# Kernel optimization log

Measured on AMD Instinct MI355X. Metric: run time of the kernel, lower is better.

The kernel has to match this reference:

```python
import jax, jax.numpy as jnp
import numpy as np

B, M, E, H, A = 32, 512, 256, 8, 64


def setup_inputs() -> dict:
    key = jax.random.key(0)
    k0, k1, k2, k3, k4 = jax.random.split(key, 5)
    s = 1.0 / np.sqrt(E)
    x = jax.random.normal(k0, (B, M, E), dtype=jnp.float32)
    Wq = jax.random.normal(k1, (E, H * A), dtype=jnp.float32) * s
    Wk = jax.random.normal(k2, (E, H * A), dtype=jnp.float32) * s
    Wv = jax.random.normal(k3, (E, H * A), dtype=jnp.float32) * s
    Wr = jax.random.normal(k4, (E, A), dtype=jnp.float32) * s
    return {"x": x, "Wq": Wq, "Wk": Wk, "Wv": Wv, "Wr": Wr}


def reference(x, Wq, Wk, Wv, Wr):
    # Faithful to the original: (B, M, H*A) tensors are view()'d directly to
    # (H, B, M, A) / (H, B, A, M) without any transpose — this mixes batch
    # into the head axis exactly as the torch code does.
    q = (x @ Wq).reshape(H, B, M, A)   # query view
    k = (x @ Wk).reshape(H, B, A, M)   # keys viewed pre-transposed
    v = (x @ Wv).reshape(H, B, M, A)
    scores = jnp.einsum('hbma,hban->hbmn', q, k)      # (H, B, M, M)
    att = jax.nn.softmax(scores, axis=-1)
    out = jnp.einsum('hbmn,hbna->hbma', att, v)       # (H, B, M, A)
    out = out.mean(axis=0)                            # head-mean -> (B, M, A)
    return jax.nn.relu(out + x @ Wr)
```

## Files before the change

### kernel.cpp

```cpp
#include <hip/hip_runtime.h>
#include <math.h>


typedef _Float16 f16;
typedef _Float16 f16x2 __attribute__((ext_vector_type(2)));
typedef _Float16 f16x4 __attribute__((ext_vector_type(4)));
typedef _Float16 f16x8 __attribute__((ext_vector_type(8)));
typedef float    f32x4 __attribute__((ext_vector_type(4)));

typedef __attribute__((address_space(1))) const void* gas_t;
typedef __attribute__((address_space(3))) void* las_t;

__device__ __forceinline__ void gload16(const void* g, void* l) {
  __builtin_amdgcn_global_load_lds((gas_t)g, (las_t)l, 16, 0, 0);
}

__global__ __launch_bounds__(256) void k_cast(const float* __restrict__ in,
                                              f16* __restrict__ out, int n4) {
  int i = blockIdx.x * 256 + threadIdx.x;
  if (i < n4) {
    f32x4 v = reinterpret_cast<const f32x4*>(in)[i];
    f16x4 h;
    h[0] = (f16)v[0]; h[1] = (f16)v[1]; h[2] = (f16)v[2]; h[3] = (f16)v[3];
    reinterpret_cast<f16x4*>(out)[i] = h;
  }
}

__global__ __launch_bounds__(256) void k_transpose_w(const float* __restrict__ Wq,
                                                     const float* __restrict__ Wk,
                                                     const float* __restrict__ Wv,
                                                     const float* __restrict__ Wr,
                                                     f16* __restrict__ Wt,
                                                     f16* __restrict__ Wrt) {
  __shared__ f16 tile[64][68];
  int b = blockIdx.x;
  const float* src; f16* dst; int r0, c0, Cin;
  if (b < 96) {
    int ws = b >> 5, rem = b & 31;
    src = (ws == 0) ? Wq : (ws == 1) ? Wk : Wv;
    dst = Wt + ws * 512 * 256;
    Cin = 512; r0 = (rem >> 3) * 64; c0 = (rem & 7) * 64;
  } else {
    src = Wr; dst = Wrt; Cin = 64; r0 = (b - 96) * 64; c0 = 0;
  }
  int t = threadIdx.x;
#pragma unroll
  for (int u = 0; u < 8; ++u) {
    int e = u * 256 + t;
    int r = e >> 5, c = (e & 31) << 1;
    const float* p = src + (long)(r0 + r) * Cin + (c0 + c);
    f16x2 v; v[0] = (f16)p[0]; v[1] = (f16)p[1];
    *reinterpret_cast<f16x2*>(&tile[r][c]) = v;
  }
  __syncthreads();
#pragma unroll
  for (int u = 0; u < 16; ++u) {
    int f = u * 256 + t;
    int cc = f >> 6, rr = f & 63;
    dst[(long)(c0 + cc) * 256 + (r0 + rr)] = tile[rr][cc];
  }
}

__global__ __launch_bounds__(256) void k_transpose(const f16* __restrict__ in,
                                                   f16* __restrict__ out,
                                                   int R_, int C_) {
  __shared__ f16 tile[64][68];
  int g = blockIdx.x;
  long gb = (long)g * R_ * C_;
  int r0 = blockIdx.y * 64, c0 = blockIdx.z * 64;
  int t = threadIdx.x;
#pragma unroll
  for (int u = 0; u < 8; ++u) {
    int e = u * 256 + t;
    int r = e >> 5, c = (e & 31) << 1;
    const f16* p = in + gb + (long)(r0 + r) * C_ + (c0 + c);
    f16x2 v; v[0] = p[0]; v[1] = p[1];
    *reinterpret_cast<f16x2*>(&tile[r][c]) = v;
  }
  __syncthreads();
#pragma unroll
  for (int u = 0; u < 16; ++u) {
    int f = u * 256 + t;
    int cc = f >> 6, rr = f & 63;
    out[gb + (long)(c0 + cc) * R_ + (r0 + rr)] = tile[rr][cc];
  }
}

template <int BN, bool F32OUT>
__global__ __launch_bounds__(256, 3) void k_gemm(const f16* __restrict__ Xh,
                                                 const f16* __restrict__ Wt,
                                                 f16* __restrict__ outH,
                                                 float* __restrict__ outF, int N) {
  __shared__ f16 Ash[128 * 64];
  __shared__ f16 Bsh[BN * 64];
  constexpr int NT = BN / 32;
  int t = threadIdx.x;
  int w = t >> 6, l = t & 63;
  int lrow = l & 15, lg = l >> 4;
  int wm = w >> 1, wn = w & 1;
  int rb = blockIdx.x * 128, cb = blockIdx.y * BN;

  f32x4 acc[4][NT] = {};

  for (int kt = 0; kt < 4; ++kt) {
    int kb = kt * 64;
    __syncthreads();
#pragma unroll
    for (int i = 0; i < 4; ++i) {
      int slot = i * 256 + t;
      int row = slot >> 3, pblk = slot & 7;
      int blk = pblk ^ (row & 7);
      gload16(Xh + (long)(rb + row) * 256 + kb + blk * 8, Ash + slot * 8);
    }
#pragma unroll
    for (int i = 0; i < BN / 32; ++i) {
      int slot = i * 256 + t;
      int row = slot >> 3, pblk = slot & 7;
      int blk = pblk ^ (row & 7);
      gload16(Wt + (long)(cb + row) * 256 + kb + blk * 8, Bsh + slot * 8);
    }
    __syncthreads();

    f16x8 af[4][2];
#pragma unroll
    for (int mi = 0; mi < 4; ++mi)
#pragma unroll
      for (int ks = 0; ks < 2; ++ks) {
        int r = 64 * wm + 16 * mi + lrow;
        af[mi][ks] = *reinterpret_cast<const f16x8*>(
            Ash + r * 64 + (((4 * ks + lg) ^ (lrow & 7)) * 8));
      }
#pragma unroll
    for (int nt = 0; nt < NT; ++nt) {
      int rB = (BN / 2) * wn + 16 * nt + lrow;
      f16x8 b0 = *reinterpret_cast<const f16x8*>(Bsh + rB * 64 + ((lg ^ (lrow & 7)) * 8));
      f16x8 b1 = *reinterpret_cast<const f16x8*>(Bsh + rB * 64 + (((4 + lg) ^ (lrow & 7)) * 8));
#pragma unroll
      for (int mi = 0; mi < 4; ++mi) {
        acc[mi][nt] = __builtin_amdgcn_mfma_f32_16x16x32_f16(af[mi][0], b0, acc[mi][nt], 0, 0, 0);
        acc[mi][nt] = __builtin_amdgcn_mfma_f32_16x16x32_f16(af[mi][1], b1, acc[mi][nt], 0, 0, 0);
      }
    }
  }
#pragma unroll
  for (int mi = 0; mi < 4; ++mi)
#pragma unroll
    for (int nt = 0; nt < NT; ++nt)
#pragma unroll
      for (int r = 0; r < 4; ++r) {
        int row = rb + 64 * wm + 16 * mi + 4 * (l >> 4) + r;
        int col = cb + (BN / 2) * wn + 16 * nt + lrow;
        float v = acc[mi][nt][r];
        if constexpr (F32OUT) {
          outF[(long)row * N + col] = v;
        } else {
          long idx = ((long)(col >> 9) << 23) + (long)row * 512 + (col & 511);
          outH[idx] = (f16)v;
        }
      }
}

__global__ __launch_bounds__(256, 3) void k_attn(const f16* __restrict__ Qh,
                                                 const f16* __restrict__ Ktg,
                                                 const f16* __restrict__ Vtg,
                                                 f16* __restrict__ Of) {
  __shared__ f16 Ksh[2][64 * 64];
  __shared__ f16 Vsh[2][64 * 64];
  __shared__ f16 Psh[4][32][72];
  int u = blockIdx.x;
  int g = (u & 7) | ((u >> 5) << 3);
  int mb = (u >> 3) & 3;
  int t = threadIdx.x, w = t >> 6, l = t & 63;
  int lrow = l & 15, lg = l >> 4, lk8 = lg * 8;
  long gp = (long)g * 32768;
  const f16* Qg = Qh + gp;
  const f16* Kg = Ktg + gp;
  const f16* Vg = Vtg + gp;
  f16* Og = Of + gp;
  int m0 = mb * 128 + w * 32;

  f16x8 qf[2][2];
#pragma unroll
  for (int mi = 0; mi < 2; ++mi)
#pragma unroll
    for (int ks = 0; ks < 2; ++ks)
      qf[mi][ks] = *reinterpret_cast<const f16x8*>(Qg + (long)(m0 + 16 * mi + lrow) * 64 + 32 * ks + lk8);

  auto stage = [&](int buf, int c) {
#pragma unroll
    for (int s = 0; s < 2; ++s) {
      int slot = s * 256 + t;
      int row = slot >> 3, pblk = slot & 7;
      gload16(Kg + (long)c * 4096 + row * 64 + ((pblk ^ (row & 7)) * 8),
              Ksh[buf] + slot * 8);
    }
#pragma unroll
    for (int s = 0; s < 2; ++s) {
      int slot = s * 256 + t;
      int a = slot >> 3, pblk = slot & 7;
      gload16(Vg + (long)a * 512 + c * 64 + ((pblk ^ (a & 7)) * 8),
              Vsh[buf] + slot * 8);
    }
  };

  f32x4 accO[2][4] = {};
  float Mx[2] = {-INFINITY, -INFINITY}, Ls[2] = {0.f, 0.f};

  stage(0, 0);
  stage(1, 1);

  for (int c = 0; c < 8; ++c) {
    int buf = c & 1;
    if (c < 7) asm volatile("s_waitcnt vmcnt(4)" ::: "memory");
    else       asm volatile("s_waitcnt vmcnt(0)" ::: "memory");
    __builtin_amdgcn_s_barrier();

    f32x4 St[2][4] = {};
    __builtin_amdgcn_s_setprio(1);
#pragma unroll
    for (int nt = 0; nt < 4; ++nt) {
      int n = 16 * nt + lrow, nb = n & 7;
      f16x8 ka = *reinterpret_cast<const f16x8*>(Ksh[buf] + n * 64 + ((lg ^ nb) * 8));
      f16x8 kb = *reinterpret_cast<const f16x8*>(Ksh[buf] + n * 64 + (((4 + lg) ^ nb) * 8));
#pragma unroll
      for (int mi = 0; mi < 2; ++mi) {
        St[mi][nt] = __builtin_amdgcn_mfma_f32_16x16x32_f16(ka, qf[mi][0], St[mi][nt], 0, 0, 0);
        St[mi][nt] = __builtin_amdgcn_mfma_f32_16x16x32_f16(kb, qf[mi][1], St[mi][nt], 0, 0, 0);
      }
    }
    __builtin_amdgcn_s_setprio(0);

    float scb[2][4];
#pragma unroll
    for (int mi = 0; mi < 2; ++mi) {
      float tm = St[mi][0][0];
#pragma unroll
      for (int nt = 0; nt < 4; ++nt)
#pragma unroll
        for (int r = 0; r < 4; ++r) tm = fmaxf(tm, St[mi][nt][r]);
      tm = fmaxf(tm, __shfl_xor(tm, 16));
      tm = fmaxf(tm, __shfl_xor(tm, 32));
      float nm = fmaxf(Mx[mi], tm);
      float sc = __expf(Mx[mi] - nm);
      Mx[mi] = nm;
      float ps = 0.f;
#pragma unroll
      for (int nt = 0; nt < 4; ++nt)
#pragma unroll
        for (int r = 0; r < 4; ++r) {
          float p = __expf(St[mi][nt][r] - nm);
          St[mi][nt][r] = p;
          ps += p;
        }
      ps += __shfl_xor(ps, 16);
      ps += __shfl_xor(ps, 32);
      Ls[mi] = Ls[mi] * sc + ps;
#pragma unroll
      for (int nt = 0; nt < 4; ++nt) {
        f16x4 p4;
        p4[0] = (f16)St[mi][nt][0]; p4[1] = (f16)St[mi][nt][1];
        p4[2] = (f16)St[mi][nt][2]; p4[3] = (f16)St[mi][nt][3];
        *reinterpret_cast<f16x4*>(&Psh[w][16 * mi + lrow][16 * nt + 4 * lg]) = p4;
      }
#pragma unroll
      for (int r = 0; r < 4; ++r) scb[mi][r] = __shfl(sc, 20 * lg + r);
    }
#pragma unroll
    for (int mi = 0; mi < 2; ++mi)
#pragma unroll
      for (int at = 0; at < 4; ++at)
#pragma unroll
        for (int r = 0; r < 4; ++r) accO[mi][at][r] *= scb[mi][r];

    __builtin_amdgcn_s_setprio(1);
#pragma unroll
    for (int ks = 0; ks < 2; ++ks) {
      f16x8 pa[2];
#pragma unroll
      for (int mi = 0; mi < 2; ++mi)
        pa[mi] = *reinterpret_cast<const f16x8*>(&Psh[w][16 * mi + lrow][32 * ks + lk8]);
#pragma unroll
      for (int at = 0; at < 4; ++at) {
        int a = 16 * at + lrow, ab = a & 7;
        f16x8 vb = *reinterpret_cast<const f16x8*>(Vsh[buf] + a * 64 + (((4 * ks + lg) ^ ab) * 8));
#pragma unroll
        for (int mi = 0; mi < 2; ++mi)
          accO[mi][at] = __builtin_amdgcn_mfma_f32_16x16x32_f16(pa[mi], vb, accO[mi][at], 0, 0, 0);
      }
    }
    __builtin_amdgcn_s_setprio(0);

    __builtin_amdgcn_s_barrier();
    if (c + 2 < 8) stage(buf, c + 2);
  }

#pragma unroll
  for (int mi = 0; mi < 2; ++mi) {
    float inv = 1.f / Ls[mi];
    float invb[4];
#pragma unroll
    for (int r = 0; r < 4; ++r) invb[r] = __shfl(inv, 20 * lg + r);
#pragma unroll
    for (int r = 0; r < 4; ++r) {
      int row = m0 + 16 * mi + 4 * lg + r;
#pragma unroll
      for (int at = 0; at < 4; ++at)
        Og[(long)row * 64 + 16 * at + lrow] = (f16)(accO[mi][at][r] * invb[r]);
    }
  }
}

__global__ __launch_bounds__(256) void k_finalize(const f16* __restrict__ Of,
                                                  const float* __restrict__ Rf,
                                                  float* __restrict__ out) {
  int i = blockIdx.x * 256 + threadIdx.x;
  f32x4 s = {};
#pragma unroll
  for (int h = 0; h < 8; ++h) {
    f16x4 o = reinterpret_cast<const f16x4*>(Of + (long)h * 1048576)[i];
#pragma unroll
    for (int j = 0; j < 4; ++j) s[j] += (float)o[j];
  }
  f32x4 r = reinterpret_cast<const f32x4*>(Rf)[i];
  f32x4 v = s * 0.125f + r;
#pragma unroll
  for (int j = 0; j < 4; ++j) v[j] = v[j] > 0.f ? v[j] : 0.f;
  reinterpret_cast<f32x4*>(out)[i] = v;
}

extern "C" void kernel_launch(void* const* d_in, const int* in_sizes, int n_in,
                              void* d_out, int out_size, void* d_ws, size_t ws_size,
                              hipStream_t stream) {
  const float* x  = (const float*)d_in[0];
  const float* Wq = (const float*)d_in[1];
  const float* Wk = (const float*)d_in[2];
  const float* Wv = (const float*)d_in[3];
  const float* Wr = (const float*)d_in[4];
  float* out = (float*)d_out;
  char* w = (char*)d_ws;

  f16*   Xh   = (f16*)(w + 0);
  f16*   Wt   = (f16*)(w + 8388608);
  f16*   Wrt  = (f16*)(w + 9175040);
  f16*   QKV  = (f16*)(w + 9207808);
  f16*   Qh   = QKV;
  f16*   Kn   = (f16*)(w + 25985024);
  f16*   Vn   = (f16*)(w + 42762240);
  f16*   Ktg  = (f16*)(w + 59539456);
  f16*   Vtg  = (f16*)(w + 76316672);
  float* Rf   = (float*)(w + 93093888);
  f16*   Of   = (f16*)(w + 25985024);

  k_cast<<<4096, 256, 0, stream>>>(x, Xh, 1048576);
  k_transpose_w<<<100, 256, 0, stream>>>(Wq, Wk, Wv, Wr, Wt, Wrt);

  k_gemm<128, false><<<dim3(128, 12), 256, 0, stream>>>(Xh, Wt, QKV, nullptr, 512);
  k_gemm<64, true><<<dim3(128, 1), 256, 0, stream>>>(Xh, Wrt, nullptr, Rf, 64);

  k_transpose<<<dim3(256, 1, 8), 256, 0, stream>>>(Kn, Ktg, 64, 512);
  k_transpose<<<dim3(256, 8, 1), 256, 0, stream>>>(Vn, Vtg, 512, 64);

  k_attn<<<1024, 256, 0, stream>>>(Qh, Ktg, Vtg, Of);
  k_finalize<<<1024, 256, 0, stream>>>(Of, Rf, out);
}
```

Measured before the change: 148.8 us.

## Fuse K/V transposes into QKV GEMM epilogue via LDS staging

Removes the two separate k_transpose launches. The QKV GEMM epilogue now writes K and V directly in the transposed layouts the attention kernel expects, staging each tile through shared memory so the global stores are 16-byte vectors. This saves two kernel launches and a full read/write round trip of K and V. The cost is a larger shared buffer and extra barriers in the GEMM, which may affect occupancy.

```diff
diff --git a/kernel.cpp b/kernel.cpp
--- a/kernel.cpp
+++ b/kernel.cpp
@@ -61,38 +61,14 @@
   }
 }
 
-__global__ __launch_bounds__(256) void k_transpose(const f16* __restrict__ in,
-                                                   f16* __restrict__ out,
-                                                   int R_, int C_) {
-  __shared__ f16 tile[64][68];
-  int g = blockIdx.x;
-  long gb = (long)g * R_ * C_;
-  int r0 = blockIdx.y * 64, c0 = blockIdx.z * 64;
-  int t = threadIdx.x;
-#pragma unroll
-  for (int u = 0; u < 8; ++u) {
-    int e = u * 256 + t;
-    int r = e >> 5, c = (e & 31) << 1;
-    const f16* p = in + gb + (long)(r0 + r) * C_ + (c0 + c);
-    f16x2 v; v[0] = p[0]; v[1] = p[1];
-    *reinterpret_cast<f16x2*>(&tile[r][c]) = v;
-  }
-  __syncthreads();
-#pragma unroll
-  for (int u = 0; u < 16; ++u) {
-    int f = u * 256 + t;
-    int cc = f >> 6, rr = f & 63;
-    out[gb + (long)(c0 + cc) * R_ + (r0 + rr)] = tile[rr][cc];
-  }
-}
-
 template <int BN, bool F32OUT>
 __global__ __launch_bounds__(256, 3) void k_gemm(const f16* __restrict__ Xh,
                                                  const f16* __restrict__ Wt,
                                                  f16* __restrict__ outH,
                                                  float* __restrict__ outF, int N) {
-  __shared__ f16 Ash[128 * 64];
-  __shared__ f16 Bsh[BN * 64];
+  __shared__ f16 smem[18432];
+  f16* Ash = smem;
+  f16* Bsh = smem + 8192;
   constexpr int NT = BN / 32;
   int t = threadIdx.x;
   int w = t >> 6, l = t & 63;
@@ -142,22 +118,83 @@
       }
     }
   }
-#pragma unroll
-  for (int mi = 0; mi < 4; ++mi)
-#pragma unroll
-    for (int nt = 0; nt < NT; ++nt)
-#pragma unroll
-      for (int r = 0; r < 4; ++r) {
-        int row = rb + 64 * wm + 16 * mi + 4 * (l >> 4) + r;
-        int col = cb + (BN / 2) * wn + 16 * nt + lrow;
-        float v = acc[mi][nt][r];
-        if constexpr (F32OUT) {
-          outF[(long)row * N + col] = v;
-        } else {
-          long idx = ((long)(col >> 9) << 23) + (long)row * 512 + (col & 511);
-          outH[idx] = (f16)v;
+
+  if constexpr (F32OUT) {
+#pragma unroll
+    for (int mi = 0; mi < 4; ++mi)
+#pragma unroll
+      for (int nt = 0; nt < NT; ++nt)
+#pragma unroll
+        for (int r = 0; r < 4; ++r) {
+          int row = rb + 64 * wm + 16 * mi + 4 * lg + r;
+          int col = cb + (BN / 2) * wn + 16 * nt + lrow;
+          outF[(long)row * N + col] = acc[mi][nt][r];
         }
-      }
+  } else {
+    int third = blockIdx.y >> 2;
+    if (third == 0) {
+#pragma unroll
+      for (int mi = 0; mi < 4; ++mi)
+#pragma unroll
+        for (int nt = 0; nt < NT; ++nt)
+#pragma unroll
+          for (int r = 0; r < 4; ++r) {
+            int row = rb + 64 * wm + 16 * mi + 4 * lg + r;
+            int col = cb + 64 * wn + 16 * nt + lrow;
+            outH[(long)row * 512 + col] = (f16)acc[mi][nt][r];
+          }
+    } else if (third == 1) {
+      int cbK = cb - 512;
+      __syncthreads();
+#pragma unroll
+      for (int mi = 0; mi < 4; ++mi)
+#pragma unroll
+        for (int nt = 0; nt < NT; ++nt)
+#pragma unroll
+          for (int r = 0; r < 4; ++r) {
+            int nl = 64 * wn + 16 * nt + lrow;
+            int a  = 16 * mi + 4 * lg + r;
+            smem[wm * 9216 + nl * 72 + a] = (f16)acc[mi][nt][r];
+          }
+      __syncthreads();
+      f16* Kt = outH + (1 << 23);
+#pragma unroll
+      for (int u = 0; u < 8; ++u) {
+        int sid = u * 256 + t;
+        int wmt = sid >> 10, rem = sid & 1023;
+        int nl = rem >> 3, a8 = rem & 7;
+        int g = (rb >> 6) + wmt;
+        int n = cbK + nl;
+        int i = ((n & 7) << 6) | (n >> 3);
+        *reinterpret_cast<f16x8*>(Kt + (long)g * 32768 + i * 64 + a8 * 8) =
+            *reinterpret_cast<const f16x8*>(smem + wmt * 9216 + nl * 72 + a8 * 8);
+      }
+    } else {
+      int j = blockIdx.y - 8;
+      __syncthreads();
+#pragma unroll
+      for (int mi = 0; mi < 4; ++mi)
+#pragma unroll
+        for (int nt = 0; nt < NT; ++nt)
+#pragma unroll
+          for (int r = 0; r < 4; ++r) {
+            int a   = 16 * nt + lrow;
+            int npl = 64 * wn + 16 * mi + 4 * lg + r;
+            smem[wm * 8704 + a * 136 + npl] = (f16)acc[mi][nt][r];
+          }
+      __syncthreads();
+      f16* Vt = outH + (2 << 23);
+#pragma unroll
+      for (int u = 0; u < 8; ++u) {
+        int sid = u * 256 + t;
+        int wmt = sid >> 10, rem = sid & 1023;
+        int a = rem >> 4, n8 = rem & 15;
+        int g = (rb >> 6) + wmt;
+        *reinterpret_cast<f16x8*>(Vt + (long)g * 32768 + a * 512 + j * 128 + n8 * 8) =
+            *reinterpret_cast<const f16x8*>(smem + wmt * 8704 + a * 136 + n8 * 8);
+      }
+    }
+  }
 }
 
 __global__ __launch_bounds__(256, 3) void k_attn(const f16* __restrict__ Qh,
@@ -342,23 +379,17 @@
   f16*   Xh   = (f16*)(w + 0);
   f16*   Wt   = (f16*)(w + 8388608);
   f16*   Wrt  = (f16*)(w + 9175040);
-  f16*   QKV  = (f16*)(w + 9207808);
-  f16*   Qh   = QKV;
-  f16*   Kn   = (f16*)(w + 25985024);
-  f16*   Vn   = (f16*)(w + 42762240);
-  f16*   Ktg  = (f16*)(w + 59539456);
-  f16*   Vtg  = (f16*)(w + 76316672);
-  float* Rf   = (float*)(w + 93093888);
-  f16*   Of   = (f16*)(w + 25985024);
+  f16*   Qh   = (f16*)(w + 9207808);
+  f16*   Ktg  = (f16*)(w + 25985024);
+  f16*   Vtg  = (f16*)(w + 42762240);
+  float* Rf   = (float*)(w + 59539456);
+  f16*   Of   = (f16*)(w + 63733760);
 
   k_cast<<<4096, 256, 0, stream>>>(x, Xh, 1048576);
   k_transpose_w<<<100, 256, 0, stream>>>(Wq, Wk, Wv, Wr, Wt, Wrt);
 
-  k_gemm<128, false><<<dim3(128, 12), 256, 0, stream>>>(Xh, Wt, QKV, nullptr, 512);
+  k_gemm<128, false><<<dim3(128, 12), 256, 0, stream>>>(Xh, Wt, Qh, nullptr, 512);
   k_gemm<64, true><<<dim3(128, 1), 256, 0, stream>>>(Xh, Wrt, nullptr, Rf, 64);
-
-  k_transpose<<<dim3(256, 1, 8), 256, 0, stream>>>(Kn, Ktg, 64, 512);
-  k_transpose<<<dim3(256, 8, 1), 256, 0, stream>>>(Vn, Vtg, 512, 64);
 
   k_attn<<<1024, 256, 0, stream>>>(Qh, Ktg, Vtg, Of);
   k_finalize<<<1024, 256, 0, stream>>>(Of, Rf, out);
```

Result: faster. 139.8 us (-6.0%).
